# Performance work log

Measured on AMD Instinct MI355X. Metric: run time of the kernel, lower is better.

The kernel has to match this reference:

```python
import jax, jax.numpy as jnp
import numpy as np

HID, HEADS, LAYERS, EDIM = 128, 2, 3, 1
HEAD_DIM = HID  # out_channels per head (concat=False -> mean over heads)
N_NODES, N_EDGES = 50000, 500000
LN_EPS = 1e-5


def _layer_norm(x, g, b):
    mu = x.mean(-1, keepdims=True)
    var = ((x - mu) ** 2).mean(-1, keepdims=True)
    return (x - mu) * jax.lax.rsqrt(var + LN_EPS) * g + b


def _transformer_conv(x, src, tgt, edge_attr, Wq, bq, Wk, bk, Wv, bv, We, Wskip, bskip):
    # PyG TransformerConv, concat=False, root_weight=True, lin_edge bias=False
    N = x.shape[0]
    E = src.shape[0]
    q = (x @ Wq + bq).reshape(N, HEADS, HEAD_DIM)
    k = (x @ Wk + bk).reshape(N, HEADS, HEAD_DIM)
    v = (x @ Wv + bv).reshape(N, HEADS, HEAD_DIM)
    e = (edge_attr @ We).reshape(E, HEADS, HEAD_DIM)          # [E,H,C]
    k_j = k[src] + e                                          # gather + edge bias
    q_i = q[tgt]
    alpha = (q_i * k_j).sum(-1) / jnp.sqrt(jnp.asarray(HEAD_DIM, x.dtype))  # [E,H]
    # scatter-softmax over incoming edges of each target node
    m = jax.ops.segment_max(alpha, tgt, num_segments=N)       # [N,H]
    a = jnp.exp(alpha - m[tgt])
    denom = jax.ops.segment_sum(a, tgt, num_segments=N)
    a = a / jnp.where(denom[tgt] > 0, denom[tgt], 1.0)
    msg = (v[src] + e) * a[..., None]                         # [E,H,C]
    out = jax.ops.segment_sum(msg, tgt, num_segments=N)       # [N,H,C]
    out = out.mean(axis=1)                                    # concat=False -> head mean
    return out + x @ Wskip + bskip                            # root/skip connection


def reference(x, edge_index, edge_attr, ln_in_g, ln_in_b,
              Wq, bq, Wk, bk, Wv, bv, We, Wskip, bskip, ln_g, ln_b):
    src, tgt = edge_index[0], edge_index[1]
    x = _layer_norm(x, ln_in_g, ln_in_b)
    for l in range(LAYERS):
        h = _transformer_conv(x, src, tgt, edge_attr,
                              Wq[l], bq[l], Wk[l], bk[l], Wv[l], bv[l],
                              We[l], Wskip[l], bskip[l])
        h = jax.nn.elu(h)
        x = _layer_norm(x + h, ln_g[l], ln_b[l])
    return x


def setup_inputs() -> dict:
    key = jax.random.key(0)
    ks = jax.random.split(key, 12)
    HC = HEADS * HEAD_DIM
    s = 1.0 / np.sqrt(HID)
    inp = {
        "x": jax.random.normal(ks[0], (N_NODES, HID), jnp.float32),
        "edge_index": jax.random.randint(ks[1], (2, N_EDGES), 0, N_NODES, jnp.int64),
        "edge_attr": jax.random.normal(ks[2], (N_EDGES, EDIM), jnp.float32),
        "ln_in_g": jnp.ones((HID,), jnp.float32),
        "ln_in_b": jnp.zeros((HID,), jnp.float32),
        "Wq": jax.random.normal(ks[3], (LAYERS, HID, HC), jnp.float32) * s,
        "bq": jnp.zeros((LAYERS, HC), jnp.float32),
        "Wk": jax.random.normal(ks[4], (LAYERS, HID, HC), jnp.float32) * s,
        "bk": jnp.zeros((LAYERS, HC), jnp.float32),
        "Wv": jax.random.normal(ks[5], (LAYERS, HID, HC), jnp.float32) * s,
        "bv": jnp.zeros((LAYERS, HC), jnp.float32),
        "We": jax.random.normal(ks[6], (LAYERS, EDIM, HC), jnp.float32),
        "Wskip": jax.random.normal(ks[7], (LAYERS, HID, HID), jnp.float32) * s,
        "bskip": jnp.zeros((LAYERS, HID), jnp.float32),
        "ln_g": jnp.ones((LAYERS, HID), jnp.float32),
        "ln_b": jnp.zeros((LAYERS, HID), jnp.float32),
    }
    return inp
```

## Files before the change

### kernel.cpp

```cpp
#include <hip/hip_runtime.h>
#include <math.h>

#define NN 50000
#define NE 500000
#define HIDS 128
#define MCOLS 896
#define NLAYERS 3

typedef __attribute__((ext_vector_type(8))) short short8;
typedef __attribute__((ext_vector_type(4))) float floatx4;
typedef _Float16 half8v __attribute__((ext_vector_type(8)));

#define GSTR 144

static __device__ __forceinline__ unsigned short f2bf(float f) {
    unsigned u = __float_as_uint(f);
    u += 0x7fffu + ((u >> 16) & 1u);
    return (unsigned short)(u >> 16);
}
static __device__ __forceinline__ unsigned short f2h(float f) {
    union { _Float16 h; unsigned short u; } c;
    c.h = (_Float16)f;
    return c.u;
}
#define DPP_ADD(v, ctrl) \
    v += __int_as_float(__builtin_amdgcn_mov_dpp(__float_as_int(v), ctrl, 0xf, 0xf, true))
static __device__ __forceinline__ float wred16(float v) {
    DPP_ADD(v, 0xB1);
    DPP_ADD(v, 0x4E);
    DPP_ADD(v, 0x124);
    DPP_ADD(v, 0x128);
    return v;
}
static __device__ __forceinline__ float wred64(float v) {
    v += __shfl_xor(v, 1, 64);
    v += __shfl_xor(v, 2, 64);
    v += __shfl_xor(v, 4, 64);
    v += __shfl_xor(v, 8, 64);
    v += __shfl_xor(v, 16, 64);
    v += __shfl_xor(v, 32, 64);
    return v;
}

__global__ __launch_bounds__(256) void eatb_count(const int* __restrict__ tgt, int* __restrict__ cnt) {
    int e = blockIdx.x * 256 + threadIdx.x;
    if (e < NE) atomicAdd(&cnt[tgt[e]], 1);
}

__global__ __launch_bounds__(256) void eatb_blocksum(const int* __restrict__ cnt, int* __restrict__ bsums) {
    __shared__ int sm[256];
    int i = blockIdx.x * 256 + threadIdx.x;
    sm[threadIdx.x] = (i < NN) ? cnt[i] : 0;
    __syncthreads();
    for (int off = 128; off > 0; off >>= 1) {
        if (threadIdx.x < off) sm[threadIdx.x] += sm[threadIdx.x + off];
        __syncthreads();
    }
    if (threadIdx.x == 0) bsums[blockIdx.x] = sm[0];
}

__global__ __launch_bounds__(256) void eatb_scanb(int* __restrict__ bsums, int nb) {
    __shared__ int sm[256];
    int t = threadIdx.x;
    int v = (t < nb) ? bsums[t] : 0;
    sm[t] = v;
    __syncthreads();
    for (int off = 1; off < 256; off <<= 1) {
        int x = (t >= off) ? sm[t - off] : 0;
        __syncthreads();
        sm[t] += x;
        __syncthreads();
    }
    if (t < nb) bsums[t] = sm[t] - v;
}

__global__ __launch_bounds__(256) void eatb_rowstart(const int* __restrict__ cnt, const int* __restrict__ bsums,
                                                     int* __restrict__ row_start) {
    __shared__ int sm[256];
    int t = threadIdx.x;
    int i = blockIdx.x * 256 + t;
    int v = (i < NN) ? cnt[i] : 0;
    sm[t] = v;
    __syncthreads();
    for (int off = 1; off < 256; off <<= 1) {
        int x = (t >= off) ? sm[t - off] : 0;
        __syncthreads();
        sm[t] += x;
        __syncthreads();
    }
    int excl = sm[t] - v + bsums[blockIdx.x];
    if (i < NN) row_start[i] = excl;
    if (i == NN - 1) row_start[NN] = excl + v;
}

__global__ __launch_bounds__(256) void eatb_scatter(const int* __restrict__ src, const int* __restrict__ tgt,
                                                    const float* __restrict__ ea, const int* __restrict__ row_start,
                                                    int* __restrict__ cursor, int2* __restrict__ csr) {
    int e = blockIdx.x * 256 + threadIdx.x;
    if (e >= NE) return;
    int t = tgt[e];
    int pos = atomicAdd(&cursor[t], 1);
    int2 val;
    val.x = src[e];
    val.y = __float_as_int(ea[e]);
    csr[row_start[t] + pos] = val;
}

__global__ __launch_bounds__(256) void eatb_packw(const float* __restrict__ Wq, const float* __restrict__ Wk,
                                                  const float* __restrict__ Wv, const float* __restrict__ Ws,
                                                  const float* __restrict__ bq, const float* __restrict__ bk,
                                                  const float* __restrict__ bv, const float* __restrict__ bs,
                                                  unsigned short* __restrict__ Wt, float* __restrict__ bcat) {
    int idx = blockIdx.x * 256 + threadIdx.x;
    const int WTOT = NLAYERS * MCOLS * HIDS;
    if (idx < WTOT) {
        int l = idx / (MCOLS * HIDS);
        int rem = idx % (MCOLS * HIDS);
        int c = rem / HIDS, k = rem % HIDS;
        float v;
        if (c < 256)      v = Wq[(l * HIDS + k) * 256 + c];
        else if (c < 512) v = Wk[(l * HIDS + k) * 256 + c - 256];
        else if (c < 768) v = Wv[(l * HIDS + k) * 256 + c - 512];
        else              v = Ws[(l * HIDS + k) * 128 + c - 768];
        Wt[idx] = f2bf(v);
    } else {
        int i2 = idx - WTOT;
        if (i2 < NLAYERS * MCOLS) {
            int l = i2 / MCOLS, c = i2 % MCOLS;
            float v;
            if (c < 256)      v = bq[l * 256 + c];
            else if (c < 512) v = bk[l * 256 + c - 256];
            else if (c < 768) v = bv[l * 256 + c - 512];
            else              v = bs[l * 128 + c - 768];
            bcat[i2] = v;
        }
    }
}

__global__ __launch_bounds__(256) void eatb_ln_in(const float* __restrict__ x, const float* __restrict__ g,
                                                  const float* __restrict__ b, float* __restrict__ xout,
                                                  unsigned short* __restrict__ xb) {
    int wid = threadIdx.x >> 6, lane = threadIdx.x & 63;
    int n = blockIdx.x * 4 + wid;
    if (n >= NN) return;
    float2 v = *(const float2*)(x + (size_t)n * HIDS + 2 * lane);
    float mu = wred64(v.x + v.y) * (1.f / 128.f);
    float cx = v.x - mu, cy = v.y - mu;
    float var = wred64(cx * cx + cy * cy) * (1.f / 128.f);
    float r = rsqrtf(var + 1e-5f);
    float2 g2 = *(const float2*)(g + 2 * lane);
    float2 b2 = *(const float2*)(b + 2 * lane);
    float2 o;
    o.x = cx * r * g2.x + b2.x;
    o.y = cy * r * g2.y + b2.y;
    *(float2*)(xout + (size_t)n * HIDS + 2 * lane) = o;
    unsigned pk = (unsigned)f2bf(o.x) | ((unsigned)f2bf(o.y) << 16);
    *(unsigned*)(xb + (size_t)n * HIDS + 2 * lane) = pk;
}

__global__ __launch_bounds__(256, 3) void eatb_gemm(const unsigned short* __restrict__ xb,
                                                    const unsigned short* __restrict__ Wt,
                                                    const float* __restrict__ bias,
                                                    unsigned short* __restrict__ qpack,
                                                    unsigned short* __restrict__ kvpack,
                                                    float* __restrict__ skipbuf) {
    __shared__ __align__(16) short As[64 * GSTR];
    __shared__ __align__(16) short Bs[64 * GSTR];
    __shared__ __align__(16) float Cs[64 * 65];

    int tid = threadIdx.x;
    int r0 = blockIdx.x * 64;
    int row = tid >> 4, ch = (tid & 15) * 8;

    #pragma unroll
    for (int p = 0; p < 4; ++p) {
        int r = row + p * 16;
        int gr = r0 + r;
        uint4 v = make_uint4(0, 0, 0, 0);
        if (gr < NN) v = *(const uint4*)(xb + (size_t)gr * HIDS + ch);
        *(uint4*)(As + r * GSTR + ch) = v;
    }
    #pragma unroll
    for (int p = 0; p < 4; ++p) {
        int r = row + p * 16;
        *(uint4*)(Bs + r * GSTR + ch) = *(const uint4*)(Wt + (size_t)r * HIDS + ch);
    }
    __syncthreads();

    int wid = tid >> 6, lane = tid & 63;
    int fr = lane & 15;
    int kq = (lane >> 4) * 8;

    for (int ci = 0; ci < 14; ++ci) {
        floatx4 acc[4] = {};
        #pragma unroll
        for (int ks = 0; ks < 4; ++ks) {
            int kof = ks * 32 + kq;
            short8 af = *(const short8*)(As + (wid * 16 + fr) * GSTR + kof);
            #pragma unroll
            for (int n = 0; n < 4; ++n) {
                short8 bf = *(const short8*)(Bs + (n * 16 + fr) * GSTR + kof);
                acc[n] = __builtin_amdgcn_mfma_f32_16x16x32_bf16(af, bf, acc[n], 0, 0, 0);
            }
        }
        #pragma unroll
        for (int n = 0; n < 4; ++n)
            #pragma unroll
            for (int rg = 0; rg < 4; ++rg)
                Cs[(wid * 16 + (lane >> 4) * 4 + rg) * 65 + n * 16 + fr] = acc[n][rg];
        __syncthreads();

        int c0 = ci * 64;
        int cl = (tid & 15) * 4;
        int C = c0 + cl;
        float4 b4 = *(const float4*)(bias + C);
        #pragma unroll
        for (int p = 0; p < 4; ++p) {
            int rr = (tid >> 4) + 16 * p;
            int gr = r0 + rr;
            if (gr >= NN) break;
            float v0 = Cs[rr * 65 + cl] + b4.x;
            float v1 = Cs[rr * 65 + cl + 1] + b4.y;
            float v2 = Cs[rr * 65 + cl + 2] + b4.z;
            float v3 = Cs[rr * 65 + cl + 3] + b4.w;
            if (C < 256) {
                ushort4 o;
                o.x = f2h(v0); o.y = f2h(v1); o.z = f2h(v2); o.w = f2h(v3);
                *(ushort4*)(qpack + (size_t)gr * 256 + C) = o;
            } else if (C < 768) {
                int u = C - 256;
                int part = u >> 7;
                int h = part & 1, isv = part >> 1;
                int d0 = u & 127;
                ushort4 o;
                o.x = f2h(v0); o.y = f2h(v1); o.z = f2h(v2); o.w = f2h(v3);
                size_t off = (size_t)gr * 512 + ((h * 16 + (d0 >> 3)) * 16) + isv * 8 + (d0 & 7);
                *(ushort4*)(kvpack + off) = o;
            } else {
                *(float4*)(skipbuf + (size_t)gr * 128 + (C - 768)) = make_float4(v0, v1, v2, v3);
            }
        }
        if (ci < 13) {
            #pragma unroll
            for (int p = 0; p < 4; ++p) {
                int r = row + p * 16;
                *(uint4*)(Bs + r * GSTR + ch) = *(const uint4*)(Wt + (size_t)((ci + 1) * 64 + r) * HIDS + ch);
            }
        }
        __syncthreads();
    }
}

__global__ __launch_bounds__(256) void eatb_attn(const unsigned short* __restrict__ qpack,
                                                 const unsigned short* __restrict__ kvpack,
                                                 const float* __restrict__ skipbuf,
                                                 const int2* __restrict__ csr, const int* __restrict__ row_start,
                                                 const float* __restrict__ Wel, const float* __restrict__ g,
                                                 const float* __restrict__ beta, const float* __restrict__ xcur,
                                                 float* __restrict__ dst, unsigned short* __restrict__ xbout) {
    int wid = threadIdx.x >> 6;
    int lane = threadIdx.x & 63;
    int n = blockIdx.x * 4 + wid;
    if (n >= NN) return;
    int slot = lane >> 5;
    int h = (lane >> 4) & 1;
    int sl = lane & 15;
    int dbase = sl * 8;

    const float rs = 0.08838834764831845f;
    const _Float16* qh16 = (const _Float16*)qpack;
    const _Float16* kvh = (const _Float16*)kvpack;

    half8v qh = *(const half8v*)(qh16 + n * 256 + h * 128 + dbase);
    float q0 = (float)qh[0] * rs, q1 = (float)qh[1] * rs, q2 = (float)qh[2] * rs, q3 = (float)qh[3] * rs;
    float q4 = (float)qh[4] * rs, q5 = (float)qh[5] * rs, q6 = (float)qh[6] * rs, q7 = (float)qh[7] * rs;
    const float* wep = Wel + h * 128 + dbase;
    float4 wea = *(const float4*)wep;
    float4 web = *(const float4*)(wep + 4);
    float qwe = wred16(q0 * wea.x + q1 * wea.y + q2 * wea.z + q3 * wea.w +
                       q4 * web.x + q5 * web.y + q6 * web.z + q7 * web.w);

    float sA = 0.f, seaA = 0.f, sB = 0.f, seaB = 0.f;
    float aA0 = 0.f, aA1 = 0.f, aA2 = 0.f, aA3 = 0.f, aA4 = 0.f, aA5 = 0.f, aA6 = 0.f, aA7 = 0.f;
    float aB0 = 0.f, aB1 = 0.f, aB2 = 0.f, aB3 = 0.f, aB4 = 0.f, aB5 = 0.f, aB6 = 0.f, aB7 = 0.f;
    int beg = row_start[n], end = row_start[n + 1];
    int nit = (end - beg + 3) >> 2;
    int lbase = (h * 16 + sl) << 4;
    for (int it = 0; it < nit; ++it) {
        int eA = beg + 4 * it + slot;
        int eB = eA + 2;
        bool vA = eA < end, vB = eB < end;
        int2 seA = csr[vA ? eA : beg];
        int2 seB = csr[vB ? eB : beg];
        int koA = (seA.x << 9) + lbase;
        int koB = (seB.x << 9) + lbase;
        half8v kqA = *(const half8v*)(kvh + koA);
        half8v vqA = *(const half8v*)(kvh + koA + 8);
        half8v kqB = *(const half8v*)(kvh + koB);
        half8v vqB = *(const half8v*)(kvh + koB + 8);
        float eaA = __int_as_float(seA.y);
        float eaB = __int_as_float(seB.y);
        float pA = q0 * (float)kqA[0] + q1 * (float)kqA[1] + q2 * (float)kqA[2] + q3 * (float)kqA[3] +
                   q4 * (float)kqA[4] + q5 * (float)kqA[5] + q6 * (float)kqA[6] + q7 * (float)kqA[7];
        float pB = q0 * (float)kqB[0] + q1 * (float)kqB[1] + q2 * (float)kqB[2] + q3 * (float)kqB[3] +
                   q4 * (float)kqB[4] + q5 * (float)kqB[5] + q6 * (float)kqB[6] + q7 * (float)kqB[7];
        pA = wred16(pA);
        pB = wred16(pB);
        float wA = vA ? __expf(pA + eaA * qwe) : 0.f;
        float wB = vB ? __expf(pB + eaB * qwe) : 0.f;
        sA += wA;
        sB += wB;
        seaA = fmaf(wA, eaA, seaA);
        seaB = fmaf(wB, eaB, seaB);
        aA0 = fmaf(wA, (float)vqA[0], aA0);  aB0 = fmaf(wB, (float)vqB[0], aB0);
        aA1 = fmaf(wA, (float)vqA[1], aA1);  aB1 = fmaf(wB, (float)vqB[1], aB1);
        aA2 = fmaf(wA, (float)vqA[2], aA2);  aB2 = fmaf(wB, (float)vqB[2], aB2);
        aA3 = fmaf(wA, (float)vqA[3], aA3);  aB3 = fmaf(wB, (float)vqB[3], aB3);
        aA4 = fmaf(wA, (float)vqA[4], aA4);  aB4 = fmaf(wB, (float)vqB[4], aB4);
        aA5 = fmaf(wA, (float)vqA[5], aA5);  aB5 = fmaf(wB, (float)vqB[5], aB5);
        aA6 = fmaf(wA, (float)vqA[6], aA6);  aB6 = fmaf(wB, (float)vqB[6], aB6);
        aA7 = fmaf(wA, (float)vqA[7], aA7);  aB7 = fmaf(wB, (float)vqB[7], aB7);
    }
    float s = sA + sB, sea = seaA + seaB;
    float a0 = aA0 + aB0, a1 = aA1 + aB1, a2 = aA2 + aB2, a3 = aA3 + aB3;
    float a4 = aA4 + aB4, a5 = aA5 + aB5, a6 = aA6 + aB6, a7 = aA7 + aB7;

    s += __shfl_xor(s, 32, 64);
    sea += __shfl_xor(sea, 32, 64);
    a0 += __shfl_xor(a0, 32, 64);
    a1 += __shfl_xor(a1, 32, 64);
    a2 += __shfl_xor(a2, 32, 64);
    a3 += __shfl_xor(a3, 32, 64);
    a4 += __shfl_xor(a4, 32, 64);
    a5 += __shfl_xor(a5, 32, 64);
    a6 += __shfl_xor(a6, 32, 64);
    a7 += __shfl_xor(a7, 32, 64);

    float inv = (s > 0.f) ? 1.f / s : 1.f;
    float sw = sea * inv;
    float o0 = a0 * inv + sw * wea.x;
    float o1 = a1 * inv + sw * wea.y;
    float o2 = a2 * inv + sw * wea.z;
    float o3 = a3 * inv + sw * wea.w;
    float o4 = a4 * inv + sw * web.x;
    float o5 = a5 * inv + sw * web.y;
    float o6 = a6 * inv + sw * web.z;
    float o7 = a7 * inv + sw * web.w;
    o0 = 0.5f * (o0 + __shfl_xor(o0, 16, 64));
    o1 = 0.5f * (o1 + __shfl_xor(o1, 16, 64));
    o2 = 0.5f * (o2 + __shfl_xor(o2, 16, 64));
    o3 = 0.5f * (o3 + __shfl_xor(o3, 16, 64));
    o4 = 0.5f * (o4 + __shfl_xor(o4, 16, 64));
    o5 = 0.5f * (o5 + __shfl_xor(o5, 16, 64));
    o6 = 0.5f * (o6 + __shfl_xor(o6, 16, 64));
    o7 = 0.5f * (o7 + __shfl_xor(o7, 16, 64));

    const float* skp = skipbuf + n * 128 + dbase;
    const float* xrp = xcur + n * 128 + dbase;
    float4 ska = *(const float4*)skp, skb = *(const float4*)(skp + 4);
    float4 xra = *(const float4*)xrp, xrb = *(const float4*)(xrp + 4);
    float y0 = o0 + ska.x, y1 = o1 + ska.y, y2 = o2 + ska.z, y3 = o3 + ska.w;
    float y4 = o4 + skb.x, y5 = o5 + skb.y, y6 = o6 + skb.z, y7 = o7 + skb.w;
    y0 = (y0 > 0.f) ? y0 : __expf(y0) - 1.f;
    y1 = (y1 > 0.f) ? y1 : __expf(y1) - 1.f;
    y2 = (y2 > 0.f) ? y2 : __expf(y2) - 1.f;
    y3 = (y3 > 0.f) ? y3 : __expf(y3) - 1.f;
    y4 = (y4 > 0.f) ? y4 : __expf(y4) - 1.f;
    y5 = (y5 > 0.f) ? y5 : __expf(y5) - 1.f;
    y6 = (y6 > 0.f) ? y6 : __expf(y6) - 1.f;
    y7 = (y7 > 0.f) ? y7 : __expf(y7) - 1.f;
    float p0 = xra.x + y0, p1 = xra.y + y1, p2 = xra.z + y2, p3 = xra.w + y3;
    float p4 = xrb.x + y4, p5 = xrb.y + y5, p6 = xrb.z + y6, p7 = xrb.w + y7;
    float mu = wred16(p0 + p1 + p2 + p3 + p4 + p5 + p6 + p7) * (1.f / 128.f);
    float c0 = p0 - mu, c1 = p1 - mu, c2 = p2 - mu, c3 = p3 - mu;
    float c4 = p4 - mu, c5 = p5 - mu, c6 = p6 - mu, c7 = p7 - mu;
    float var = wred16(c0 * c0 + c1 * c1 + c2 * c2 + c3 * c3 +
                       c4 * c4 + c5 * c5 + c6 * c6 + c7 * c7) * (1.f / 128.f);
    float r = rsqrtf(var + 1e-5f);
    if (lane < 16) {
        const float* gp = g + dbase;
        const float* bp = beta + dbase;
        float4 ga = *(const float4*)gp, gb = *(const float4*)(gp + 4);
        float4 ba = *(const float4*)bp, bb = *(const float4*)(bp + 4);
        float4 oa, ob;
        oa.x = c0 * r * ga.x + ba.x; oa.y = c1 * r * ga.y + ba.y;
        oa.z = c2 * r * ga.z + ba.z; oa.w = c3 * r * ga.w + ba.w;
        ob.x = c4 * r * gb.x + bb.x; ob.y = c5 * r * gb.y + bb.y;
        ob.z = c6 * r * gb.z + bb.z; ob.w = c7 * r * gb.w + bb.w;
        float* dp = dst + n * 128 + dbase;
        *(float4*)dp = oa;
        *(float4*)(dp + 4) = ob;
        if (xbout) {
            uint4 pk;
            pk.x = (unsigned)f2bf(oa.x) | ((unsigned)f2bf(oa.y) << 16);
            pk.y = (unsigned)f2bf(oa.z) | ((unsigned)f2bf(oa.w) << 16);
            pk.z = (unsigned)f2bf(ob.x) | ((unsigned)f2bf(ob.y) << 16);
            pk.w = (unsigned)f2bf(ob.z) | ((unsigned)f2bf(ob.w) << 16);
            *(uint4*)(xbout + n * 128 + dbase) = pk;
        }
    }
}

extern "C" void kernel_launch(void* const* d_in, const int* in_sizes, int n_in,
                              void* d_out, int out_size, void* d_ws, size_t ws_size,
                              hipStream_t stream) {
    const float* x       = (const float*)d_in[0];
    const int*   ei      = (const int*)d_in[1];
    const float* eattr   = (const float*)d_in[2];
    const float* ln_in_g = (const float*)d_in[3];
    const float* ln_in_b = (const float*)d_in[4];
    const float* Wq = (const float*)d_in[5];
    const float* bq = (const float*)d_in[6];
    const float* Wk = (const float*)d_in[7];
    const float* bk = (const float*)d_in[8];
    const float* Wv = (const float*)d_in[9];
    const float* bv = (const float*)d_in[10];
    const float* We = (const float*)d_in[11];
    const float* Ws = (const float*)d_in[12];
    const float* bs = (const float*)d_in[13];
    const float* ln_g = (const float*)d_in[14];
    const float* ln_b = (const float*)d_in[15];
    float* out = (float*)d_out;

    char* p = (char*)d_ws;
    auto carve = [&](size_t bytes) {
        char* r = p;
        p += (bytes + 255) & ~(size_t)255;
        return (void*)r;
    };
    int*  cursor    = (int*)carve((size_t)NN * 4);
    int*  row_start = (int*)carve((size_t)(NN + 1) * 4);
    int*  bsums     = (int*)carve(1024);
    int2* csr       = (int2*)carve((size_t)NE * 8);
    unsigned short* WcatT = (unsigned short*)carve((size_t)NLAYERS * MCOLS * HIDS * 2);
    float* bcat     = (float*)carve((size_t)NLAYERS * MCOLS * 4);
    float* xcur     = (float*)carve((size_t)NN * HIDS * 4);
    unsigned short* qpack  = (unsigned short*)carve((size_t)NN * 256 * 2);
    unsigned short* kvpack = (unsigned short*)carve((size_t)NN * 512 * 2);
    float* skipbuf  = (float*)carve((size_t)NN * HIDS * 4);
    unsigned short* xb = (unsigned short*)carve((size_t)NN * HIDS * 2);

    const int NB_N = (NN + 255) / 256;
    const int NB_E = (NE + 255) / 256;
    const int NODE_BLOCKS = (NN + 3) / 4;

    hipMemsetAsync(cursor, 0, (size_t)NN * 4, stream);
    eatb_count<<<NB_E, 256, 0, stream>>>(ei + NE, cursor);
    eatb_blocksum<<<NB_N, 256, 0, stream>>>(cursor, bsums);
    eatb_scanb<<<1, 256, 0, stream>>>(bsums, NB_N);
    eatb_rowstart<<<NB_N, 256, 0, stream>>>(cursor, bsums, row_start);
    hipMemsetAsync(cursor, 0, (size_t)NN * 4, stream);
    eatb_scatter<<<NB_E, 256, 0, stream>>>(ei, ei + NE, eattr, row_start, cursor, csr);

    {
        int tot = NLAYERS * MCOLS * HIDS + NLAYERS * MCOLS;
        eatb_packw<<<(tot + 255) / 256, 256, 0, stream>>>(Wq, Wk, Wv, Ws, bq, bk, bv, bs, WcatT, bcat);
    }

    eatb_ln_in<<<NODE_BLOCKS, 256, 0, stream>>>(x, ln_in_g, ln_in_b, xcur, xb);

    const int GEMM_BLOCKS = (NN + 63) / 64;
    for (int l = 0; l < NLAYERS; ++l) {
        eatb_gemm<<<GEMM_BLOCKS, 256, 0, stream>>>(xb, WcatT + (size_t)l * MCOLS * HIDS,
                                                   bcat + (size_t)l * MCOLS, qpack, kvpack, skipbuf);
        float* dst = (l == NLAYERS - 1) ? out : xcur;
        unsigned short* xbo = (l == NLAYERS - 1) ? nullptr : xb;
        eatb_attn<<<NODE_BLOCKS, 256, 0, stream>>>(qpack, kvpack, skipbuf, csr, row_start,
                                                   We + (size_t)l * 256, ln_g + (size_t)l * 128,
                                                   ln_b + (size_t)l * 128, xcur, dst, xbo);
    }
    (void)in_sizes; (void)n_in; (void)out_size; (void)ws_size;
}
```

Baseline: 589.6 us.

## Load GEMM operands directly into registers, store skip in fp16, simplify KV layout

The GEMM kernel no longer stages A and B tiles in shared memory. A fragments are loaded once into registers and B fragments are read straight from global memory/cache per MFMA, which shrinks LDS use and raises the occupancy hint to 4. The skip projection output is stored as fp16 instead of fp32, halving its write and read traffic. The K/V interleaved layout becomes plain contiguous K then V per node, and the attention gather offsets change to match. The trade-offs are more global/L2 reads of the weights and reduced precision on the skip path.

```diff
diff --git a/kernel.cpp b/kernel.cpp
--- a/kernel.cpp
+++ b/kernel.cpp
@@ -10,8 +10,6 @@
 typedef __attribute__((ext_vector_type(8))) short short8;
 typedef __attribute__((ext_vector_type(4))) float floatx4;
 typedef _Float16 half8v __attribute__((ext_vector_type(8)));
-
-#define GSTR 144
 
 static __device__ __forceinline__ unsigned short f2bf(float f) {
     unsigned u = __float_as_uint(f);
@@ -158,102 +156,76 @@
     *(unsigned*)(xb + (size_t)n * HIDS + 2 * lane) = pk;
 }
 
-__global__ __launch_bounds__(256, 3) void eatb_gemm(const unsigned short* __restrict__ xb,
+__global__ __launch_bounds__(256, 4) void eatb_gemm(const unsigned short* __restrict__ xb,
                                                     const unsigned short* __restrict__ Wt,
                                                     const float* __restrict__ bias,
                                                     unsigned short* __restrict__ qpack,
                                                     unsigned short* __restrict__ kvpack,
-                                                    float* __restrict__ skipbuf) {
-    __shared__ __align__(16) short As[64 * GSTR];
-    __shared__ __align__(16) short Bs[64 * GSTR];
-    __shared__ __align__(16) float Cs[64 * 65];
+                                                    unsigned short* __restrict__ skipbuf) {
+    __shared__ __align__(16) float Cs[64 * 68];
 
     int tid = threadIdx.x;
     int r0 = blockIdx.x * 64;
-    int row = tid >> 4, ch = (tid & 15) * 8;
-
-    #pragma unroll
-    for (int p = 0; p < 4; ++p) {
-        int r = row + p * 16;
-        int gr = r0 + r;
-        uint4 v = make_uint4(0, 0, 0, 0);
-        if (gr < NN) v = *(const uint4*)(xb + (size_t)gr * HIDS + ch);
-        *(uint4*)(As + r * GSTR + ch) = v;
-    }
-    #pragma unroll
-    for (int p = 0; p < 4; ++p) {
-        int r = row + p * 16;
-        *(uint4*)(Bs + r * GSTR + ch) = *(const uint4*)(Wt + (size_t)r * HIDS + ch);
-    }
-    __syncthreads();
-
     int wid = tid >> 6, lane = tid & 63;
     int fr = lane & 15;
     int kq = (lane >> 4) * 8;
 
+    int ar = r0 + wid * 16 + fr;
+    bool aok = ar < NN;
+    const unsigned short* aptr = xb + (size_t)(aok ? ar : 0) * HIDS;
+    short8 afk[4];
+    #pragma unroll
+    for (int ks = 0; ks < 4; ++ks) afk[ks] = *(const short8*)(aptr + ks * 32 + kq);
+    if (!aok) {
+        short8 z = {};
+        afk[0] = z; afk[1] = z; afk[2] = z; afk[3] = z;
+    }
+
+    int cl = (tid & 15) * 4;
     for (int ci = 0; ci < 14; ++ci) {
+        int c0 = ci * 64;
         floatx4 acc[4] = {};
         #pragma unroll
-        for (int ks = 0; ks < 4; ++ks) {
-            int kof = ks * 32 + kq;
-            short8 af = *(const short8*)(As + (wid * 16 + fr) * GSTR + kof);
+        for (int n = 0; n < 4; ++n) {
+            const unsigned short* bptr = Wt + (size_t)(c0 + n * 16 + fr) * HIDS;
             #pragma unroll
-            for (int n = 0; n < 4; ++n) {
-                short8 bf = *(const short8*)(Bs + (n * 16 + fr) * GSTR + kof);
-                acc[n] = __builtin_amdgcn_mfma_f32_16x16x32_bf16(af, bf, acc[n], 0, 0, 0);
+            for (int ks = 0; ks < 4; ++ks) {
+                short8 bf = *(const short8*)(bptr + ks * 32 + kq);
+                acc[n] = __builtin_amdgcn_mfma_f32_16x16x32_bf16(afk[ks], bf, acc[n], 0, 0, 0);
             }
         }
         #pragma unroll
         for (int n = 0; n < 4; ++n)
             #pragma unroll
             for (int rg = 0; rg < 4; ++rg)
-                Cs[(wid * 16 + (lane >> 4) * 4 + rg) * 65 + n * 16 + fr] = acc[n][rg];
-        __syncthreads();
-
-        int c0 = ci * 64;
-        int cl = (tid & 15) * 4;
+                Cs[(wid * 16 + (lane >> 4) * 4 + rg) * 68 + n * 16 + fr] = acc[n][rg];
+        __syncthreads();
+
         int C = c0 + cl;
         float4 b4 = *(const float4*)(bias + C);
         #pragma unroll
         for (int p = 0; p < 4; ++p) {
             int rr = (tid >> 4) + 16 * p;
             int gr = r0 + rr;
-            if (gr >= NN) break;
-            float v0 = Cs[rr * 65 + cl] + b4.x;
-            float v1 = Cs[rr * 65 + cl + 1] + b4.y;
-            float v2 = Cs[rr * 65 + cl + 2] + b4.z;
-            float v3 = Cs[rr * 65 + cl + 3] + b4.w;
-            if (C < 256) {
+            if (gr < NN) {
+                float4 cv = *(const float4*)(Cs + rr * 68 + cl);
                 ushort4 o;
-                o.x = f2h(v0); o.y = f2h(v1); o.z = f2h(v2); o.w = f2h(v3);
-                *(ushort4*)(qpack + (size_t)gr * 256 + C) = o;
-            } else if (C < 768) {
-                int u = C - 256;
-                int part = u >> 7;
-                int h = part & 1, isv = part >> 1;
-                int d0 = u & 127;
-                ushort4 o;
-                o.x = f2h(v0); o.y = f2h(v1); o.z = f2h(v2); o.w = f2h(v3);
-                size_t off = (size_t)gr * 512 + ((h * 16 + (d0 >> 3)) * 16) + isv * 8 + (d0 & 7);
-                *(ushort4*)(kvpack + off) = o;
-            } else {
-                *(float4*)(skipbuf + (size_t)gr * 128 + (C - 768)) = make_float4(v0, v1, v2, v3);
+                o.x = f2h(cv.x + b4.x);
+                o.y = f2h(cv.y + b4.y);
+                o.z = f2h(cv.z + b4.z);
+                o.w = f2h(cv.w + b4.w);
+                if (C < 256)      *(ushort4*)(qpack + (size_t)gr * 256 + C) = o;
+                else if (C < 768) *(ushort4*)(kvpack + (size_t)gr * 512 + (C - 256)) = o;
+                else              *(ushort4*)(skipbuf + (size_t)gr * 128 + (C - 768)) = o;
             }
         }
-        if (ci < 13) {
-            #pragma unroll
-            for (int p = 0; p < 4; ++p) {
-                int r = row + p * 16;
-                *(uint4*)(Bs + r * GSTR + ch) = *(const uint4*)(Wt + (size_t)((ci + 1) * 64 + r) * HIDS + ch);
-            }
-        }
         __syncthreads();
     }
 }
 
 __global__ __launch_bounds__(256) void eatb_attn(const unsigned short* __restrict__ qpack,
                                                  const unsigned short* __restrict__ kvpack,
-                                                 const float* __restrict__ skipbuf,
+                                                 const unsigned short* __restrict__ skipbuf,
                                                  const int2* __restrict__ csr, const int* __restrict__ row_start,
                                                  const float* __restrict__ Wel, const float* __restrict__ g,
                                                  const float* __restrict__ beta, const float* __restrict__ xcur,
@@ -285,7 +257,7 @@
     float aB0 = 0.f, aB1 = 0.f, aB2 = 0.f, aB3 = 0.f, aB4 = 0.f, aB5 = 0.f, aB6 = 0.f, aB7 = 0.f;
     int beg = row_start[n], end = row_start[n + 1];
     int nit = (end - beg + 3) >> 2;
-    int lbase = (h * 16 + sl) << 4;
+    int lbase = (h << 7) + (sl << 3);
     for (int it = 0; it < nit; ++it) {
         int eA = beg + 4 * it + slot;
         int eB = eA + 2;
@@ -295,9 +267,9 @@
         int koA = (seA.x << 9) + lbase;
         int koB = (seB.x << 9) + lbase;
         half8v kqA = *(const half8v*)(kvh + koA);
-        half8v vqA = *(const half8v*)(kvh + koA + 8);
+        half8v vqA = *(const half8v*)(kvh + koA + 256);
         half8v kqB = *(const half8v*)(kvh + koB);
-        half8v vqB = *(const half8v*)(kvh + koB + 8);
+        half8v vqB = *(const half8v*)(kvh + koB + 256);
         float eaA = __int_as_float(seA.y);
         float eaB = __int_as_float(seB.y);
         float pA = q0 * (float)kqA[0] + q1 * (float)kqA[1] + q2 * (float)kqA[2] + q3 * (float)kqA[3] +
@@ -355,12 +327,12 @@
     o6 = 0.5f * (o6 + __shfl_xor(o6, 16, 64));
     o7 = 0.5f * (o7 + __shfl_xor(o7, 16, 64));
 
-    const float* skp = skipbuf + n * 128 + dbase;
+    const _Float16* skp = (const _Float16*)skipbuf + n * 128 + dbase;
+    half8v skh = *(const half8v*)skp;
     const float* xrp = xcur + n * 128 + dbase;
-    float4 ska = *(const float4*)skp, skb = *(const float4*)(skp + 4);
     float4 xra = *(const float4*)xrp, xrb = *(const float4*)(xrp + 4);
-    float y0 = o0 + ska.x, y1 = o1 + ska.y, y2 = o2 + ska.z, y3 = o3 + ska.w;
-    float y4 = o4 + skb.x, y5 = o5 + skb.y, y6 = o6 + skb.z, y7 = o7 + skb.w;
+    float y0 = o0 + (float)skh[0], y1 = o1 + (float)skh[1], y2 = o2 + (float)skh[2], y3 = o3 + (float)skh[3];
+    float y4 = o4 + (float)skh[4], y5 = o5 + (float)skh[5], y6 = o6 + (float)skh[6], y7 = o7 + (float)skh[7];
     y0 = (y0 > 0.f) ? y0 : __expf(y0) - 1.f;
     y1 = (y1 > 0.f) ? y1 : __expf(y1) - 1.f;
     y2 = (y2 > 0.f) ? y2 : __expf(y2) - 1.f;
@@ -437,7 +409,7 @@
     float* xcur     = (float*)carve((size_t)NN * HIDS * 4);
     unsigned short* qpack  = (unsigned short*)carve((size_t)NN * 256 * 2);
     unsigned short* kvpack = (unsigned short*)carve((size_t)NN * 512 * 2);
-    float* skipbuf  = (float*)carve((size_t)NN * HIDS * 4);
+    unsigned short* skipbuf = (unsigned short*)carve((size_t)NN * HIDS * 2);
     unsigned short* xb = (unsigned short*)carve((size_t)NN * HIDS * 2);
 
     const int NB_N = (NN + 255) / 256;
```

Result: slower. 749.2 us (+27.1%).
